# Performance work log

Measured on AMD Instinct MI355X. Metric: run time of the kernel, lower is better.

## Reference

```python
import jax, jax.numpy as jnp
import numpy as np

N, E = 100000, 1600000
IN_DIM, H, D = 128, 4, 32
ALPHA = 0.2  # leaky relu negative slope


def setup_inputs() -> dict:
    key = jax.random.key(0)
    k1, k2, k3, k4, k5, k6 = jax.random.split(key, 6)
    return {
        "inputs": jax.random.normal(k1, (N, IN_DIM), dtype=jnp.float32),
        "src": jax.random.randint(k2, (E,), 0, N, dtype=jnp.int32),
        "dst": jax.random.randint(k3, (E,), 0, N, dtype=jnp.int32),
        "fc_w": jax.random.normal(k4, (IN_DIM, H * D), dtype=jnp.float32) * (1.414 / np.sqrt(IN_DIM)),
        "attn_l": jax.random.normal(k5, (D,), dtype=jnp.float32) * 0.1,
        "attn_r": jax.random.normal(k6, (D,), dtype=jnp.float32) * 0.1,
    }


def reference(inputs, src, dst, fc_w, attn_l, attn_r):
    # fc + reshape to (N, H, D); feat_drop is identity (p=0)
    ft = (inputs @ fc_w).reshape(N, H, D)
    # attn_l/attn_r are (1,1,D) in torch -> broadcast over heads
    a1 = jnp.einsum("nhd,d->nh", ft, attn_l)  # (N, H)
    a2 = jnp.einsum("nhd,d->nh", ft, attn_r)  # (N, H)
    # per-edge logits; original keeps ONLY head-0 scores after edge_softmax
    # (scores[:, 0, :].unsqueeze(1)), so we only need head 0 here.
    e = jax.nn.leaky_relu(a1[src, 0] + a2[dst, 0], ALPHA)  # (E,)
    # numerically-stable segment softmax over destination nodes
    emax = jax.ops.segment_max(e, dst, num_segments=N)
    ex = jnp.exp(e - emax[dst])
    denom = jax.ops.segment_sum(ex, dst, num_segments=N)
    a = ex / denom[dst]  # (E,) broadcast to all heads
    # u_mul_e + sum aggregation; attn_drop is identity (p=0)
    msg = ft[src] * a[:, None, None]  # (E, H, D)
    out = jax.ops.segment_sum(msg, dst, num_segments=N)  # (N, H, D)
    return out
```

## Files before the change

kernel.cpp:

```cpp
#include <hip/hip_runtime.h>


#define ALPHA 0.2f
#define NBLK 512
#define BBITS 8
#define BSIZE 256
#define CAP 5120
#define ESLOTS 1024

typedef __attribute__((ext_vector_type(8))) short bf16x8;
typedef __attribute__((ext_vector_type(8))) unsigned short u16x8;
typedef __attribute__((ext_vector_type(4))) float f32x4;
typedef __attribute__((ext_vector_type(2))) float f32x2;

__device__ __forceinline__ unsigned short f2bf(float f) {
    unsigned u = __float_as_uint(f);
    unsigned r = (u + 0x7FFFu + ((u >> 16) & 1u)) >> 16;
    return (unsigned short)r;
}

__global__ __launch_bounds__(256) void front_kernel(
        const float* __restrict__ A, const float* __restrict__ W,
        const float* __restrict__ attn_l, const float* __restrict__ attn_r,
        unsigned short* __restrict__ ftb,
        float* __restrict__ s_l, float* __restrict__ s_r, int N, int GB,
        const int* __restrict__ dst, unsigned* __restrict__ bh,
        int E, int nbucket, int slice) {
    __shared__ char smem[32768];
    const int tid = threadIdx.x;

    if (blockIdx.x >= (unsigned)GB) {
        unsigned* cnt = (unsigned*)smem;
        for (int i = tid; i < nbucket; i += 256) cnt[i] = 0u;
        __syncthreads();
        const int b = blockIdx.x - GB;
        int s0 = b * slice, s1 = min(s0 + slice, E);
        for (int i = s0 + tid; i < s1; i += 256)
            atomicAdd(&cnt[((unsigned)dst[i]) >> BBITS], 1u);
        __syncthreads();
        for (int k = tid; k < nbucket; k += 256)
            bh[(size_t)k * NBLK + b] = cnt[k];
        return;
    }

    u16x8* W_lds = (u16x8*)smem;
    const int block_row = blockIdx.x * 64;

    for (int i = tid; i < 2048; i += 256) {
        int n = i & 127, c = i >> 7;
        u16x8 v;
        #pragma unroll
        for (int j = 0; j < 8; ++j) v[j] = f2bf(W[(c * 8 + j) * 128 + n]);
        W_lds[n * 16 + (c ^ (n & 7))] = v;
    }

    const int wv = tid >> 6;
    const int lane = tid & 63;
    const int lm = lane & 15;
    const int quad = lane >> 4;
    const int am = block_row + wv * 16 + lm;
    const bool rowok = (am < N);

    bf16x8 a_frag[4];
    #pragma unroll
    for (int ks = 0; ks < 4; ++ks) {
        int c = ks * 4 + quad;
        float4 v0 = make_float4(0.f, 0.f, 0.f, 0.f), v1 = v0;
        if (rowok) {
            const float4* p = (const float4*)(A + (size_t)am * 128 + c * 8);
            v0 = p[0]; v1 = p[1];
        }
        u16x8 u;
        u[0] = f2bf(v0.x); u[1] = f2bf(v0.y); u[2] = f2bf(v0.z); u[3] = f2bf(v0.w);
        u[4] = f2bf(v1.x); u[5] = f2bf(v1.y); u[6] = f2bf(v1.z); u[7] = f2bf(v1.w);
        a_frag[ks] = *(const bf16x8*)&u;
    }
    __syncthreads();

    f32x4 acc[8];
    #pragma unroll
    for (int t = 0; t < 8; ++t) acc[t] = (f32x4)(0.f);

    #pragma unroll
    for (int ks = 0; ks < 4; ++ks) {
        int c = ks * 4 + quad;
        #pragma unroll
        for (int t = 0; t < 8; ++t) {
            int n = t * 16 + lm;
            bf16x8 bf = *(const bf16x8*)&W_lds[n * 16 + (c ^ (n & 7))];
            acc[t] = __builtin_amdgcn_mfma_f32_16x16x32_bf16(a_frag[ks], bf, acc[t], 0, 0, 0);
        }
    }

    {
        float al0 = attn_l[lm], al1 = attn_l[16 + lm];
        float ar0 = attn_r[lm], ar1 = attn_r[16 + lm];
        #pragma unroll
        for (int r = 0; r < 4; ++r) {
            float pl = acc[0][r] * al0 + acc[1][r] * al1;
            float pr = acc[0][r] * ar0 + acc[1][r] * ar1;
            #pragma unroll
            for (int mask = 1; mask < 16; mask <<= 1) {
                pl += __shfl_xor(pl, mask, 64);
                pr += __shfl_xor(pr, mask, 64);
            }
            if (lm == 0) {
                int row = block_row + wv * 16 + quad * 4 + r;
                if (row < N) { s_l[row] = pl; s_r[row] = pr; }
            }
        }
    }

    __syncthreads();
    unsigned short* C_lds = (unsigned short*)smem;
    #pragma unroll
    for (int t = 0; t < 8; ++t) {
        #pragma unroll
        for (int r = 0; r < 4; ++r) {
            int mrow = wv * 16 + quad * 4 + r;
            C_lds[mrow * 128 + t * 16 + lm] = f2bf(acc[t][r]);
        }
    }
    __syncthreads();
    for (int l = tid; l < 1024; l += 256) {
        int m = l >> 4, c = l & 15;
        int row = block_row + m;
        if (row < N)
            *(u16x8*)(ftb + (size_t)row * 128 + c * 8) = *(const u16x8*)&C_lds[m * 128 + c * 8];
    }
}

__global__ __launch_bounds__(256) void scan1_kernel(const unsigned* __restrict__ counts,
                                                    unsigned* __restrict__ S,
                                                    unsigned* __restrict__ partials, int M) {
    __shared__ unsigned sh[256];
    const int tid = threadIdx.x;
    const int base = blockIdx.x * 1024 + tid * 4;
    unsigned v[4];
    unsigned s = 0;
    #pragma unroll
    for (int k = 0; k < 4; ++k) {
        int idx = base + k;
        v[k] = (idx < M) ? counts[idx] : 0u;
        s += v[k];
    }
    sh[tid] = s;
    __syncthreads();
    for (int off = 1; off < 256; off <<= 1) {
        unsigned t = (tid >= off) ? sh[tid - off] : 0u;
        __syncthreads();
        sh[tid] += t;
        __syncthreads();
    }
    if (tid == 255) partials[blockIdx.x] = sh[255];
    unsigned run = (tid == 0) ? 0u : sh[tid - 1];
    #pragma unroll
    for (int k = 0; k < 4; ++k) {
        int idx = base + k;
        if (idx < M) S[idx] = run;
        run += v[k];
    }
}

__device__ __forceinline__ void local_pscan(const unsigned* __restrict__ partials,
                                            unsigned* pscan, int NB, int tid) {
    unsigned pv = (tid < NB) ? partials[tid] : 0u;
    pscan[tid] = pv;
    __syncthreads();
    for (int off = 1; off < 256; off <<= 1) {
        unsigned t = (tid >= off) ? pscan[tid - off] : 0u;
        __syncthreads();
        pscan[tid] += t;
        __syncthreads();
    }
    unsigned excl = (tid == 0) ? 0u : pscan[tid - 1];
    __syncthreads();
    pscan[tid] = excl;
    __syncthreads();
}

__global__ __launch_bounds__(256) void bscatter_kernel(
        const int* __restrict__ src, const int* __restrict__ dst,
        const float* __restrict__ s_l, const float* __restrict__ s_r,
        const unsigned* __restrict__ S, const unsigned* __restrict__ partials,
        uint2* __restrict__ staged, int E, int nbucket, int slice, int NB) {
    __shared__ unsigned pscan[256];
    __shared__ unsigned basel[512];
    __shared__ unsigned cur[512];
    const int b = blockIdx.x;
    const int tid = threadIdx.x;
    local_pscan(partials, pscan, NB, tid);
    for (int k = tid; k < nbucket; k += 256) {
        unsigned idx = (unsigned)k * NBLK + b;
        basel[k] = S[idx] + pscan[idx >> 10];
        cur[k] = 0u;
    }
    __syncthreads();
    int s0 = b * slice, s1 = min(s0 + slice, E);
    for (int i = s0 + tid; i < s1; i += 256) {
        int s = src[i], d = dst[i];
        unsigned k = ((unsigned)d) >> BBITS;
        float x = s_l[s] + s_r[d];
        float e = (x > 0.f) ? x : ALPHA * x;
        unsigned pos = basel[k] + atomicAdd(&cur[k], 1u);
        staged[pos] = make_uint2((unsigned)s | (((unsigned)d & (BSIZE - 1)) << 20),
                                 __float_as_uint(e));
    }
}

__global__ __launch_bounds__(256) void bsort_kernel(
        uint2* __restrict__ staged, const unsigned* __restrict__ S,
        const unsigned* __restrict__ partials,
        unsigned* __restrict__ offsets, int N, int E, int nbucket, int NB) {
    __shared__ uint2 rec[CAP];
    __shared__ unsigned pscan[256];
    __shared__ unsigned cnt[BSIZE], incl[BSIZE], cur[BSIZE];
    const int k = blockIdx.x;
    const int t = threadIdx.x;
    local_pscan(partials, pscan, NB, t);
    unsigned idx0 = (unsigned)k * NBLK;
    unsigned gstart = S[idx0] + pscan[idx0 >> 10];
    unsigned gend = (k + 1 == nbucket) ? (unsigned)E
                                       : (S[idx0 + NBLK] + pscan[(idx0 + NBLK) >> 10]);
    int n = (int)(gend - gstart);
    if (n > CAP) n = CAP;

    cnt[t] = 0u;
    __syncthreads();
    for (int i = t; i < n; i += 256)
        atomicAdd(&cnt[staged[gstart + i].x >> 20], 1u);
    __syncthreads();
    incl[t] = cnt[t];
    __syncthreads();
    for (int off = 1; off < 256; off <<= 1) {
        unsigned u = (t >= off) ? incl[t - off] : 0u;
        __syncthreads();
        incl[t] += u;
        __syncthreads();
    }
    cur[t] = 0u;
    __syncthreads();
    for (int i = t; i < n; i += 256) {
        uint2 r = staged[gstart + i];
        unsigned dl = r.x >> 20;
        unsigned p = incl[dl] - cnt[dl] + atomicAdd(&cur[dl], 1u);
        rec[p] = r;
    }
    __syncthreads();
    int d = k * BSIZE + t;
    if (d < N) {
        int b0 = (int)(incl[t] - cnt[t]);
        int c = (int)cnt[t];
        float m = -1e30f;
        for (int j = 0; j < c; ++j) m = fmaxf(m, __uint_as_float(rec[b0 + j].y));
        float sum = 0.f;
        for (int j = 0; j < c; ++j) sum += __expf(__uint_as_float(rec[b0 + j].y) - m);
        float rden = (c > 0) ? 1.f / sum : 0.f;
        for (int j = 0; j < c; ++j) {
            float a = __expf(__uint_as_float(rec[b0 + j].y) - m) * rden;
            rec[b0 + j].y = __float_as_uint(a);
        }
        offsets[d] = gstart + incl[t];
    }
    __syncthreads();
    for (int i = t; i < n; i += 256) {
        uint2 r = rec[i];
        staged[gstart + i] = make_uint2(r.x & 0xFFFFFu, r.y);
    }
}

__global__ __launch_bounds__(256) void aggregate_kernel(
        const uint2* __restrict__ edata, const unsigned* __restrict__ offsets,
        const unsigned short* __restrict__ ftb, float* __restrict__ out, int N) {
    __shared__ uint2 elds[ESLOTS];
    const int wv = threadIdx.x >> 6;
    const int lane = threadIdx.x & 63;
    const int eh = lane >> 4;
    const int j  = lane & 15;
    const int db = blockIdx.x * 4;
    const int d = db + wv;

    const unsigned bstart = (db == 0) ? 0u : offsets[db - 1];
    const unsigned bend = offsets[min(db + 3, N - 1)];
    unsigned start = 0u, end = 0u;
    if (d < N) {
        start = (d == 0) ? 0u : offsets[d - 1];
        end = offsets[d];
    }

    f32x2 acc2[4];
    #pragma unroll
    for (int p = 0; p < 4; ++p) acc2[p] = (f32x2)(0.f);

    for (unsigned cbase = bstart; cbase < bend; cbase += ESLOTS) {
        const unsigned cn = min((unsigned)ESLOTS, bend - cbase);
        __syncthreads();
        for (unsigned i = threadIdx.x; i < cn; i += 256)
            elds[i] = edata[cbase + i];
        __syncthreads();
        const unsigned lo = (start > cbase) ? start : cbase;
        const unsigned hi = (end < cbase + cn) ? end : (cbase + cn);
        for (unsigned e = lo; e < hi; e += 16) {
            unsigned i0 = e + eh, i1 = e + 4 + eh, i2 = e + 8 + eh, i3 = e + 12 + eh;
            uint2 e0 = (i0 < hi) ? elds[i0 - cbase] : make_uint2(0u, 0u);
            uint2 e1 = (i1 < hi) ? elds[i1 - cbase] : make_uint2(0u, 0u);
            uint2 e2 = (i2 < hi) ? elds[i2 - cbase] : make_uint2(0u, 0u);
            uint2 e3 = (i3 < hi) ? elds[i3 - cbase] : make_uint2(0u, 0u);
            uint4 q0 = *(const uint4*)(ftb + ((unsigned)(e0.x << 7) + (j << 3)));
            uint4 q1 = *(const uint4*)(ftb + ((unsigned)(e1.x << 7) + (j << 3)));
            uint4 q2 = *(const uint4*)(ftb + ((unsigned)(e2.x << 7) + (j << 3)));
            uint4 q3 = *(const uint4*)(ftb + ((unsigned)(e3.x << 7) + (j << 3)));
            float a0 = __uint_as_float(e0.y);
            float a1 = __uint_as_float(e1.y);
            float a2 = __uint_as_float(e2.y);
            float a3 = __uint_as_float(e3.y);
            const unsigned* w0 = (const unsigned*)&q0;
            const unsigned* w1 = (const unsigned*)&q1;
            const unsigned* w2 = (const unsigned*)&q2;
            const unsigned* w3 = (const unsigned*)&q3;
            #pragma unroll
            for (int p = 0; p < 4; ++p) {
                f32x2 v0 = { __uint_as_float(w0[p] << 16), __uint_as_float(w0[p] & 0xFFFF0000u) };
                f32x2 v1 = { __uint_as_float(w1[p] << 16), __uint_as_float(w1[p] & 0xFFFF0000u) };
                f32x2 v2 = { __uint_as_float(w2[p] << 16), __uint_as_float(w2[p] & 0xFFFF0000u) };
                f32x2 v3 = { __uint_as_float(w3[p] << 16), __uint_as_float(w3[p] & 0xFFFF0000u) };
                acc2[p] += v0 * a0;
                acc2[p] += v1 * a1;
                acc2[p] += v2 * a2;
                acc2[p] += v3 * a3;
            }
        }
    }
    float acc[8];
    #pragma unroll
    for (int p = 0; p < 4; ++p) { acc[2 * p] = acc2[p][0]; acc[2 * p + 1] = acc2[p][1]; }
    #pragma unroll
    for (int p = 0; p < 8; ++p) {
        acc[p] += __shfl_xor(acc[p], 16, 64);
        acc[p] += __shfl_xor(acc[p], 32, 64);
    }
    if (d < N && eh == 0) {
        float4* op = (float4*)(out + (size_t)d * 128 + j * 8);
        op[0] = make_float4(acc[0], acc[1], acc[2], acc[3]);
        op[1] = make_float4(acc[4], acc[5], acc[6], acc[7]);
    }
}

static inline size_t align256(size_t x) { return (x + 255) & ~(size_t)255; }

extern "C" void kernel_launch(void* const* d_in, const int* in_sizes, int n_in,
                              void* d_out, int out_size, void* d_ws, size_t ws_size,
                              hipStream_t stream) {
    const float* inputs = (const float*)d_in[0];
    const int*   src    = (const int*)d_in[1];
    const int*   dst    = (const int*)d_in[2];
    const float* fc_w   = (const float*)d_in[3];
    const float* attn_l = (const float*)d_in[4];
    const float* attn_r = (const float*)d_in[5];
    float* out = (float*)d_out;

    const int N = in_sizes[0] / 128;
    const int E = in_sizes[1];
    const int nbucket = (N + BSIZE - 1) / BSIZE;
    const int M = nbucket * NBLK;
    const int NB1 = (M + 1023) / 1024;
    const int slice = (E + NBLK - 1) / NBLK;
    const int GB = (N + 63) / 64;

    char* w = (char*)d_ws;
    unsigned short* ftb = (unsigned short*)w;  w += align256((size_t)N * 128 * 2);
    float*    s_l      = (float*)w;     w += align256((size_t)N * 4);
    float*    s_r      = (float*)w;     w += align256((size_t)N * 4);
    unsigned* bh       = (unsigned*)w;  w += align256((size_t)M * 4);
    unsigned* S        = (unsigned*)w;  w += align256((size_t)M * 4);
    unsigned* partials = (unsigned*)w;  w += align256(1024 * 4);
    unsigned* offsets  = (unsigned*)w;  w += align256((size_t)N * 4);
    uint2*    staged   = (uint2*)w;     w += align256((size_t)E * 8);

    front_kernel<<<GB + NBLK, 256, 0, stream>>>(inputs, fc_w, attn_l, attn_r,
                                                ftb, s_l, s_r, N, GB,
                                                dst, bh, E, nbucket, slice);
    scan1_kernel<<<NB1, 256, 0, stream>>>(bh, S, partials, M);
    bscatter_kernel<<<NBLK, 256, 0, stream>>>(src, dst, s_l, s_r, S, partials,
                                              staged, E, nbucket, slice, NB1);
    bsort_kernel<<<nbucket, 256, 0, stream>>>(staged, S, partials, offsets,
                                              N, E, nbucket, NB1);
    aggregate_kernel<<<(N + 3) / 4, 256, 0, stream>>>(staged, offsets, ftb, out, N);
}
```

Measured before the change: 247.6 us.

## Halve destination bucket size and double scatter blocks with wider partial scan

Shrinks destination buckets from 256 to 128 nodes and doubles the number of scatter blocks to 1024. This gives twice as many sort blocks with smaller shared-memory footprints, which should raise occupancy and shorten each block's per-node softmax stage. The partial-sum scan now handles up to 1024 partials with four per thread. The trade-offs are that only half the threads do per-node work in the sort kernel, and the scatter kernel holds larger basel/cur tables.

```diff
diff --git a/kernel.cpp b/kernel.cpp
--- a/kernel.cpp
+++ b/kernel.cpp
@@ -2,10 +2,10 @@
 
 
 #define ALPHA 0.2f
-#define NBLK 512
-#define BBITS 8
-#define BSIZE 256
-#define CAP 5120
+#define NBLK 1024
+#define BBITS 7
+#define BSIZE 128
+#define CAP 2816
 #define ESLOTS 1024
 
 typedef __attribute__((ext_vector_type(8))) short bf16x8;
@@ -162,20 +162,32 @@
     }
 }
 
-__device__ __forceinline__ void local_pscan(const unsigned* __restrict__ partials,
-                                            unsigned* pscan, int NB, int tid) {
-    unsigned pv = (tid < NB) ? partials[tid] : 0u;
-    pscan[tid] = pv;
+__device__ __forceinline__ void local_pscan4(const unsigned* __restrict__ partials,
+                                             unsigned* pscan, unsigned* tsh,
+                                             int NB, int tid) {
+    unsigned v[4];
+    unsigned s = 0;
+    #pragma unroll
+    for (int k = 0; k < 4; ++k) {
+        int idx = tid * 4 + k;
+        v[k] = (idx < NB) ? partials[idx] : 0u;
+        s += v[k];
+    }
+    tsh[tid] = s;
     __syncthreads();
     for (int off = 1; off < 256; off <<= 1) {
-        unsigned t = (tid >= off) ? pscan[tid - off] : 0u;
-        __syncthreads();
-        pscan[tid] += t;
-        __syncthreads();
-    }
-    unsigned excl = (tid == 0) ? 0u : pscan[tid - 1];
-    __syncthreads();
-    pscan[tid] = excl;
+        unsigned t = (tid >= off) ? tsh[tid - off] : 0u;
+        __syncthreads();
+        tsh[tid] += t;
+        __syncthreads();
+    }
+    unsigned run = (tid == 0) ? 0u : tsh[tid - 1];
+    #pragma unroll
+    for (int k = 0; k < 4; ++k) {
+        int idx = tid * 4 + k;
+        if (idx < NB) pscan[idx] = run;
+        run += v[k];
+    }
     __syncthreads();
 }
 
@@ -184,12 +196,13 @@
         const float* __restrict__ s_l, const float* __restrict__ s_r,
         const unsigned* __restrict__ S, const unsigned* __restrict__ partials,
         uint2* __restrict__ staged, int E, int nbucket, int slice, int NB) {
-    __shared__ unsigned pscan[256];
-    __shared__ unsigned basel[512];
-    __shared__ unsigned cur[512];
+    __shared__ unsigned pscan[1024];
+    __shared__ unsigned tsh[256];
+    __shared__ unsigned basel[1024];
+    __shared__ unsigned cur[1024];
     const int b = blockIdx.x;
     const int tid = threadIdx.x;
-    local_pscan(partials, pscan, NB, tid);
+    local_pscan4(partials, pscan, tsh, NB, tid);
     for (int k = tid; k < nbucket; k += 256) {
         unsigned idx = (unsigned)k * NBLK + b;
         basel[k] = S[idx] + pscan[idx >> 10];
@@ -213,11 +226,12 @@
         const unsigned* __restrict__ partials,
         unsigned* __restrict__ offsets, int N, int E, int nbucket, int NB) {
     __shared__ uint2 rec[CAP];
-    __shared__ unsigned pscan[256];
+    __shared__ unsigned pscan[1024];
+    __shared__ unsigned tsh[256];
     __shared__ unsigned cnt[BSIZE], incl[BSIZE], cur[BSIZE];
     const int k = blockIdx.x;
     const int t = threadIdx.x;
-    local_pscan(partials, pscan, NB, t);
+    local_pscan4(partials, pscan, tsh, NB, t);
     unsigned idx0 = (unsigned)k * NBLK;
     unsigned gstart = S[idx0] + pscan[idx0 >> 10];
     unsigned gend = (k + 1 == nbucket) ? (unsigned)E
@@ -225,21 +239,19 @@
     int n = (int)(gend - gstart);
     if (n > CAP) n = CAP;
 
-    cnt[t] = 0u;
+    if (t < BSIZE) { cnt[t] = 0u; cur[t] = 0u; }
     __syncthreads();
     for (int i = t; i < n; i += 256)
         atomicAdd(&cnt[staged[gstart + i].x >> 20], 1u);
     __syncthreads();
-    incl[t] = cnt[t];
-    __syncthreads();
-    for (int off = 1; off < 256; off <<= 1) {
-        unsigned u = (t >= off) ? incl[t - off] : 0u;
-        __syncthreads();
-        incl[t] += u;
-        __syncthreads();
-    }
-    cur[t] = 0u;
-    __syncthreads();
+    if (t < BSIZE) incl[t] = cnt[t];
+    __syncthreads();
+    for (int off = 1; off < BSIZE; off <<= 1) {
+        unsigned u = (t < BSIZE && t >= off) ? incl[t - off] : 0u;
+        __syncthreads();
+        if (t < BSIZE) incl[t] += u;
+        __syncthreads();
+    }
     for (int i = t; i < n; i += 256) {
         uint2 r = staged[gstart + i];
         unsigned dl = r.x >> 20;
@@ -248,7 +260,7 @@
     }
     __syncthreads();
     int d = k * BSIZE + t;
-    if (d < N) {
+    if (t < BSIZE && d < N) {
         int b0 = (int)(incl[t] - cnt[t]);
         int c = (int)cnt[t];
         float m = -1e30f;
```

Result: slower. 255.8 us (+3.3%).
